# Kernel tuning notes

Hardware: AMD Instinct MI355X
Metric: run time of the kernel (lower is better)

Reference implementation:

```python
import jax, jax.numpy as jnp
import numpy as np

B, S, H, NH = 4, 2048, 1024, 16
HD = H // NH

def setup_inputs() -> dict:
    key = jax.random.key(0)
    ks = jax.random.split(key, 11)
    std = 1.0 / np.sqrt(H)
    inp = {
        'query': jax.random.normal(ks[0], (B, S, H), dtype=jnp.float32),
        'key':   jax.random.normal(ks[1], (B, S, H), dtype=jnp.float32),
        'value': jax.random.normal(ks[2], (B, S, H), dtype=jnp.float32),
        'Wq': jax.random.uniform(ks[3], (H, H), jnp.float32, -std, std),
        'bq': jax.random.uniform(ks[4], (H,), jnp.float32, -std, std),
        'Wk': jax.random.uniform(ks[5], (H, H), jnp.float32, -std, std),
        'bk': jax.random.uniform(ks[6], (H,), jnp.float32, -std, std),
        'Wv': jax.random.uniform(ks[7], (H, H), jnp.float32, -std, std),
        'bv': jax.random.uniform(ks[8], (H,), jnp.float32, -std, std),
        'Wo': jax.random.uniform(ks[9], (H, H), jnp.float32, -std, std),
        'bo': jax.random.uniform(ks[10], (H,), jnp.float32, -std, std),
    }
    return inp

def reference(query, key, value, Wq, bq, Wk, bk, Wv, bv, Wo, bo):
    def split_heads(x):  # [B,S,H] -> [B,NH,S,HD]
        return x.reshape(B, -1, NH, HD).transpose(0, 2, 1, 3)
    Q = split_heads(query @ Wq.T + bq)
    K = split_heads(key @ Wk.T + bk)
    V = split_heads(value @ Wv.T + bv)
    scores = jnp.einsum('bhqd,bhkd->bhqk', Q, K) / np.sqrt(HD).astype(np.float32)
    weights = jax.nn.softmax(scores, axis=-1)
    attn = jnp.einsum('bhqk,bhkd->bhqd', weights, V)  # [B,NH,S,HD]
    attn = attn.transpose(0, 2, 1, 3).reshape(B, -1, H)
    return attn @ Wo.T + bo
```

## Files before the change

### kernel.cpp

```cpp
#include <hip/hip_runtime.h>
#include <hip/hip_bf16.h>

typedef __attribute__((ext_vector_type(4)))  float f32x4;
typedef __attribute__((ext_vector_type(16))) float f32x16;
typedef __attribute__((ext_vector_type(8)))  short bf16x8;
typedef __attribute__((ext_vector_type(4)))  short bf16x4;

#define DEVI static __device__ __forceinline__
#define WAITV(N) asm volatile("s_waitcnt vmcnt(" #N ")" ::: "memory")
#define BAR() __builtin_amdgcn_s_barrier()
#define SCHEDB() __builtin_amdgcn_sched_barrier(0)

constexpr int Bn = 4, Sn = 2048, Hn = 1024, NHn = 16, HDn = 64;
constexpr int Kn = 1024, Nn = 1024;
constexpr float QSCALE = 0.18033688011112042f;

DEVI unsigned short f2bf(float x) {
    union { float f; unsigned u; } v; v.f = x;
    unsigned r = v.u + 0x7fffu + ((v.u >> 16) & 1u);
    return (unsigned short)(r >> 16);
}

DEVI f32x4 mfma16(bf16x8 a, bf16x8 b, f32x4 c) {
    return __builtin_amdgcn_mfma_f32_16x16x32_bf16(a, b, c, 0, 0, 0);
}
DEVI f32x16 mfma32(bf16x8 a, bf16x8 b, f32x16 c) {
    return __builtin_amdgcn_mfma_f32_32x32x16_bf16(a, b, c, 0, 0, 0);
}
DEVI unsigned cvt_pk_bf16(float lo, float hi) {
    unsigned r;
    asm("v_cvt_pk_bf16_f32 %0, %1, %2" : "=v"(r) : "v"(lo), "v"(hi));
    return r;
}
DEVI void pl32swap(unsigned &a, unsigned &b) {
    asm("v_permlane32_swap_b32 %0, %1" : "+v"(a), "+v"(b));
}
DEVI float exp2_raw(float x) { return __builtin_amdgcn_exp2f(x); }

typedef const __attribute__((address_space(1))) void* gas1_t;
typedef __attribute__((address_space(3))) void* gas3_t;

__global__ void convert_w_kernel(const float* __restrict__ w0, const float* __restrict__ w1,
                                 const float* __restrict__ w2, const float* __restrict__ w3,
                                 unsigned short* __restrict__ out)
{
    int mat = blockIdx.x >> 10;
    int i4  = ((blockIdx.x & 1023) << 8) + threadIdx.x;
    const float* w = mat == 0 ? w0 : mat == 1 ? w1 : mat == 2 ? w2 : w3;
    f32x4 v = *reinterpret_cast<const f32x4*>(w + (size_t)i4 * 4);
    union { unsigned u[2]; bf16x4 s; } pk;
    pk.u[0] = cvt_pk_bf16(v[0], v[1]);
    pk.u[1] = cvt_pk_bf16(v[2], v[3]);
    *reinterpret_cast<bf16x4*>(out + (((size_t)mat) << 20) + (size_t)i4 * 4) = pk.s;
}

__global__ __launch_bounds__(256, 2)
void out_proj_kernel(const unsigned short* __restrict__ Aw, const unsigned short* __restrict__ Bw,
                     const float* __restrict__ bias, float* __restrict__ Out)
{
    __shared__ __align__(16) unsigned short As[128 * 32];
    __shared__ __align__(16) unsigned short Bs[128 * 32];

    const int tid = threadIdx.x;
    const int wid = tid >> 6, lane = tid & 63;
    const int lhi = lane >> 4, llo = lane & 15;
    const int bid = blockIdx.x;
    const int sid = (bid & 7) * 64 + (bid >> 3);
    const int bx = sid & 7, by = sid >> 3;
    const int brow = by * 128, bcol = bx * 128;
    const int wr = wid >> 1, wc = wid & 1;

    f32x4 acc[4][4] = {};

    for (int kt = 0; kt < Kn / 32; ++kt) {
        __syncthreads();
        #pragma unroll
        for (int r = 0; r < 2; ++r) {
            int lin = r * 256 + tid;
            int row = lin >> 2, kc = (lin & 3) * 8;
            __builtin_amdgcn_global_load_lds(
                (gas1_t)(Bw + (size_t)(bcol + row) * Kn + kt * 32 + kc),
                (gas3_t)(Bs + (size_t)(r * 256 + wid * 64) * 8), 16, 0, 0);
        }
        #pragma unroll
        for (int r = 0; r < 2; ++r) {
            int lin = r * 256 + tid;
            int row = lin >> 2, kc = (lin & 3) * 8;
            __builtin_amdgcn_global_load_lds(
                (gas1_t)(Aw + (size_t)(brow + row) * Kn + kt * 32 + kc),
                (gas3_t)(As + (size_t)(r * 256 + wid * 64) * 8), 16, 0, 0);
        }
        __syncthreads();

        bf16x8 a[4], b[4];
        #pragma unroll
        for (int m = 0; m < 4; ++m)
            a[m] = *reinterpret_cast<const bf16x8*>(As + (wr * 64 + m * 16 + llo) * 32 + lhi * 8);
        #pragma unroll
        for (int n = 0; n < 4; ++n)
            b[n] = *reinterpret_cast<const bf16x8*>(Bs + (wc * 64 + n * 16 + llo) * 32 + lhi * 8);
        #pragma unroll
        for (int m = 0; m < 4; ++m)
            #pragma unroll
            for (int n = 0; n < 4; ++n)
                acc[m][n] = mfma16(a[m], b[n], acc[m][n]);
    }

    #pragma unroll
    for (int m = 0; m < 4; ++m)
        #pragma unroll
        for (int n = 0; n < 4; ++n) {
            const int col  = bcol + wc * 64 + n * 16 + llo;
            const int row0 = brow + wr * 64 + m * 16 + lhi * 4;
            const float bv = bias[col];
            #pragma unroll
            for (int r = 0; r < 4; ++r)
                Out[(size_t)(row0 + r) * Nn + col] = acc[m][n][r] + bv;
        }
}

__global__ __launch_bounds__(256, 2)
void qkv_proj_kernel(const float* __restrict__ xq, const float* __restrict__ xk,
                     const float* __restrict__ xv, const unsigned short* __restrict__ Wb,
                     const float* __restrict__ bq, const float* __restrict__ bk,
                     const float* __restrict__ bv,
                     unsigned short* __restrict__ Qw, unsigned short* __restrict__ Kw,
                     unsigned short* __restrict__ Vw)
{
    __shared__ __align__(16) unsigned short As[2][128 * 32];
    __shared__ __align__(16) unsigned short Bs[2][128 * 32];

    const int z = blockIdx.z;
    const float* A           = z == 0 ? xq : z == 1 ? xk : xv;
    const unsigned short* W  = Wb + (((size_t)z) << 20);
    const float* bias        = z == 0 ? bq : z == 1 ? bk : bv;
    unsigned short* Out      = z == 0 ? Qw : z == 1 ? Kw : Vw;
    const float scale        = z == 0 ? QSCALE : 1.0f;

    const int tid = threadIdx.x;
    const int wid = tid >> 6, lane = tid & 63;
    const int lhi = lane >> 4, llo = lane & 15;
    const int bid = blockIdx.x;
    const int sid = (bid & 7) * 64 + (bid >> 3);
    const int bx = sid & 7, by = sid >> 3;
    const int brow = by * 128, bcol = bx * 128;
    const int wr = wid >> 1, wc = wid & 1;

    f32x4 acc[4][4] = {};

    auto issueA = [&](f32x4 (&ar)[4], int kt) {
        #pragma unroll
        for (int r = 0; r < 4; ++r) {
            int lin = r * 256 + tid;
            int row = lin >> 3, kc = (lin & 7) * 4;
            ar[r] = *reinterpret_cast<const f32x4*>(A + (size_t)(brow + row) * Kn + kt * 32 + kc);
        }
    };
    auto stageB = [&](int buf, int kt) {
        #pragma unroll
        for (int r = 0; r < 2; ++r) {
            int lin = r * 256 + tid;
            int row = lin >> 2, kc = (lin & 3) * 8;
            __builtin_amdgcn_global_load_lds(
                (gas1_t)(W + (size_t)(bcol + row) * Kn + kt * 32 + kc),
                (gas3_t)(Bs[buf] + (size_t)(r * 256 + wid * 64) * 8), 16, 0, 0);
        }
    };
    auto writeA = [&](int buf, f32x4 (&ar)[4]) {
        #pragma unroll
        for (int r = 0; r < 4; ++r) {
            int lin = r * 256 + tid;
            int row = lin >> 3, kc = (lin & 7) * 4;
            union { unsigned u[2]; bf16x4 s; } pk;
            pk.u[0] = cvt_pk_bf16(ar[r][0], ar[r][1]);
            pk.u[1] = cvt_pk_bf16(ar[r][2], ar[r][3]);
            *reinterpret_cast<bf16x4*>(As[buf] + row * 32 + kc) = pk.s;
        }
    };
    auto compute = [&](int buf) {
        bf16x8 a[4], b[4];
        #pragma unroll
        for (int m = 0; m < 4; ++m)
            a[m] = *reinterpret_cast<const bf16x8*>(As[buf] + (wr * 64 + m * 16 + llo) * 32 + lhi * 8);
        #pragma unroll
        for (int n = 0; n < 4; ++n)
            b[n] = *reinterpret_cast<const bf16x8*>(Bs[buf] + (wc * 64 + n * 16 + llo) * 32 + lhi * 8);
        #pragma unroll
        for (int m = 0; m < 4; ++m)
            #pragma unroll
            for (int n = 0; n < 4; ++n)
                acc[m][n] = mfma16(a[m], b[n], acc[m][n]);
    };

    constexpr int NKT = Kn / 32;
    f32x4 ar0[4], ar1[4];

    issueA(ar0, 0);
    stageB(0, 0);
    writeA(0, ar0);
    __syncthreads();

    for (int kt = 0; kt < NKT; kt += 2) {
        issueA(ar1, kt + 1);
        stageB(1, kt + 1);
        compute(0);
        writeA(1, ar1);
        __syncthreads();
        if (kt + 2 < NKT) { issueA(ar0, kt + 2); stageB(0, kt + 2); }
        compute(1);
        if (kt + 2 < NKT) writeA(0, ar0);
        __syncthreads();
    }

    #pragma unroll
    for (int m = 0; m < 4; ++m) {
        #pragma unroll
        for (int n = 0; n < 4; ++n) {
            const int col  = bcol + wc * 64 + n * 16 + llo;
            const int row0 = brow + wr * 64 + m * 16 + lhi * 4;
            const float bv = bias[col];
            const int hh = col >> 6, d = col & 63;
            if (z != 2) {
                unsigned short* O = (unsigned short*)Out;
                #pragma unroll
                for (int r = 0; r < 4; ++r) {
                    int rowm = row0 + r;
                    int bb = rowm >> 11, ss = rowm & 2047;
                    O[((((size_t)bb * NHn + hh) * Sn + ss) << 6) + d] =
                        f2bf((acc[m][n][r] + bv) * scale);
                }
            } else {
                unsigned short* O = (unsigned short*)Out;
                const int bb = row0 >> 11, ss = row0 & 2047;
                union { unsigned u[2]; bf16x4 s; } pk;
                pk.u[0] = cvt_pk_bf16(acc[m][n][0] + bv, acc[m][n][1] + bv);
                pk.u[1] = cvt_pk_bf16(acc[m][n][2] + bv, acc[m][n][3] + bv);
                *reinterpret_cast<bf16x4*>(O + (((size_t)bb * NHn + hh) * HDn + d) * Sn + ss) = pk.s;
            }
        }
    }
}

__global__ __launch_bounds__(256, 2)
void attn_kernel(const unsigned short* __restrict__ Q, const unsigned short* __restrict__ K,
                 const unsigned short* __restrict__ Vt, unsigned short* __restrict__ On)
{
    __shared__ __align__(16) unsigned short LDST[3 * 8192];

    const int tid = threadIdx.x;
    const int wid = tid >> 6, lane = tid & 63;
    const int l31 = lane & 31, h = lane >> 5;
    const int bid = blockIdx.x;
    const int sid = (bid & 7) * 64 + (bid >> 3);
    const int bh = sid >> 3;
    const int qt = sid & 7;
    const int q0 = qt * 256 + wid * 64;

    const unsigned short* Qb = Q + (size_t)bh * Sn * HDn;
    const unsigned short* Kb = K + (size_t)bh * Sn * HDn;
    const unsigned short* Vb = Vt + (size_t)bh * HDn * Sn;

    int koff[2], voff[2];
    #pragma unroll
    for (int r = 0; r < 2; ++r) {
        int lin = (r * 256 + tid) * 16;
        int row = lin >> 7, colb = lin & 127;
        int scolb = colb ^ ((row & 7) << 4);
        koff[r] = row * HDn + (scolb >> 1);
        voff[r] = row * Sn + (scolb >> 1);
    }

    auto stage = [&](int bufEl, int key0) {
        #pragma unroll
        for (int r = 0; r < 2; ++r)
            __builtin_amdgcn_global_load_lds((gas1_t)(Kb + koff[r] + key0 * HDn),
                (gas3_t)(LDST + bufEl + r * 2048 + wid * 512), 16, 0, 0);
        #pragma unroll
        for (int r = 0; r < 2; ++r)
            __builtin_amdgcn_global_load_lds((gas1_t)(Vb + voff[r] + key0),
                (gas3_t)(LDST + bufEl + 4096 + r * 2048 + wid * 512), 16, 0, 0);
    };
    auto rdT = [&](int byteoff) -> bf16x8 {
        return *reinterpret_cast<const bf16x8*>((const char*)LDST + byteoff);
    };
    const int lrow = l31 * 128;
    const int lswz = (l31 & 7) << 4;

    bf16x8 qfA[4], qfB[4];
    #pragma unroll
    for (int sd = 0; sd < 4; ++sd) {
        qfA[sd] = *reinterpret_cast<const bf16x8*>(Qb + (size_t)(q0 + l31) * HDn + sd * 16 + h * 8);
        qfB[sd] = *reinterpret_cast<const bf16x8*>(Qb + (size_t)(q0 + 32 + l31) * HDn + sd * 16 + h * 8);
    }

    f32x16 oA0 = {}, oA1 = {}, oB0 = {}, oB1 = {};
    float lA = 0.f, lB = 0.f;

    auto body = [&](int base) {
        bf16x8 ka0[4], ka1[4];
        #pragma unroll
        for (int sd = 0; sd < 4; ++sd) {
            int la = lrow + ((sd * 32 + h * 16) ^ lswz);
            ka0[sd] = rdT(base + la);
            ka1[sd] = rdT(base + 4096 + la);
        }
        f32x16 sA0 = {}, sA1 = {}, sB0 = {}, sB1 = {};
        __builtin_amdgcn_s_setprio(1);
        #pragma unroll
        for (int sd = 0; sd < 4; ++sd) sA0 = mfma32(ka0[sd], qfA[sd], sA0);
        #pragma unroll
        for (int sd = 0; sd < 4; ++sd) sA1 = mfma32(ka1[sd], qfA[sd], sA1);
        #pragma unroll
        for (int sd = 0; sd < 4; ++sd) sB0 = mfma32(ka0[sd], qfB[sd], sB0);
        #pragma unroll
        for (int sd = 0; sd < 4; ++sd) sB1 = mfma32(ka1[sd], qfB[sd], sB1);
        __builtin_amdgcn_s_setprio(0);

        bf16x8 va0[4], va1[4];
        #pragma unroll
        for (int S = 0; S < 4; ++S) {
            int la = lrow + ((S * 32 + h * 16) ^ lswz);
            va0[S] = rdT(base + 8192 + la);
            va1[S] = rdT(base + 8192 + 4096 + la);
        }

        #pragma unroll
        for (int r = 0; r < 16; ++r) {
            sA0[r] = exp2_raw(sA0[r]); sA1[r] = exp2_raw(sA1[r]);
            sB0[r] = exp2_raw(sB0[r]); sB1[r] = exp2_raw(sB1[r]);
        }

        {
            float sa[16], sb[16];
            #pragma unroll
            for (int r = 0; r < 16; ++r) { sa[r] = sA0[r] + sA1[r]; sb[r] = sB0[r] + sB1[r]; }
            #pragma unroll
            for (int st = 8; st > 0; st >>= 1)
                #pragma unroll
                for (int r = 0; r < 8; ++r)
                    if (r < st) { sa[r] += sa[r + st]; sb[r] += sb[r + st]; }
            lA += sa[0];
            lB += sb[0];
        }

        unsigned WpA[2][4][2], WpB[2][4][2];
        #pragma unroll
        for (int R = 0; R < 4; ++R) {
            WpA[0][R][0] = cvt_pk_bf16(sA0[4 * R],     sA0[4 * R + 1]);
            WpA[0][R][1] = cvt_pk_bf16(sA0[4 * R + 2], sA0[4 * R + 3]);
            WpA[1][R][0] = cvt_pk_bf16(sA1[4 * R],     sA1[4 * R + 1]);
            WpA[1][R][1] = cvt_pk_bf16(sA1[4 * R + 2], sA1[4 * R + 3]);
            WpB[0][R][0] = cvt_pk_bf16(sB0[4 * R],     sB0[4 * R + 1]);
            WpB[0][R][1] = cvt_pk_bf16(sB0[4 * R + 2], sB0[4 * R + 3]);
            WpB[1][R][0] = cvt_pk_bf16(sB1[4 * R],     sB1[4 * R + 1]);
            WpB[1][R][1] = cvt_pk_bf16(sB1[4 * R + 2], sB1[4 * R + 3]);
        }

        #pragma unroll
        for (int kc = 0; kc < 2; ++kc) {
            #pragma unroll
            for (int sp = 0; sp < 2; ++sp) {
                const int S = kc * 2 + sp;
                unsigned a0 = WpA[kc][2 * sp][0], a2 = WpA[kc][2 * sp + 1][0];
                unsigned a1 = WpA[kc][2 * sp][1], a3 = WpA[kc][2 * sp + 1][1];
                pl32swap(a0, a2);
                pl32swap(a1, a3);
                union { unsigned u[4]; bf16x8 v; } pbA;
                pbA.u[0] = a0; pbA.u[1] = a1; pbA.u[2] = a2; pbA.u[3] = a3;
                unsigned b0 = WpB[kc][2 * sp][0], b2 = WpB[kc][2 * sp + 1][0];
                unsigned b1 = WpB[kc][2 * sp][1], b3 = WpB[kc][2 * sp + 1][1];
                pl32swap(b0, b2);
                pl32swap(b1, b3);
                union { unsigned u[4]; bf16x8 v; } pbB;
                pbB.u[0] = b0; pbB.u[1] = b1; pbB.u[2] = b2; pbB.u[3] = b3;
                __builtin_amdgcn_s_setprio(1);
                oA0 = mfma32(va0[S], pbA.v, oA0);
                oA1 = mfma32(va1[S], pbA.v, oA1);
                oB0 = mfma32(va0[S], pbB.v, oB0);
                oB1 = mfma32(va1[S], pbB.v, oB1);
                __builtin_amdgcn_s_setprio(0);
            }
        }
    };

    constexpr int NT = Sn / 64;
    stage(0, 0);
    int ec = 0, en = 8192, e2 = 16384;
    for (int n = 0; n < NT; ++n) {
        if (n + 1 < NT) {
            stage(en, (n + 1) * 64);
            WAITV(4);
        } else {
            WAITV(0);
        }
        BAR(); SCHEDB();
        body(ec * 2);
        int t = ec; ec = en; en = e2; e2 = t;
    }

    lA += __shfl_xor(lA, 32, 64);
    lB += __shfl_xor(lB, 32, 64);
    const float invA = 1.f / lA, invB = 1.f / lB;
    const int b = bh >> 4, hh = bh & 15;
    unsigned short* OrowA = On + ((size_t)b * Sn + (q0 + l31))      * Hn + hh * 64;
    unsigned short* OrowB = On + ((size_t)b * Sn + (q0 + 32 + l31)) * Hn + hh * 64;
    #pragma unroll
    for (int g = 0; g < 4; ++g) {
        union { unsigned u[2]; bf16x4 s; } pA0, pA1, pB0, pB1;
        pA0.u[0] = cvt_pk_bf16(oA0[4 * g] * invA,     oA0[4 * g + 1] * invA);
        pA0.u[1] = cvt_pk_bf16(oA0[4 * g + 2] * invA, oA0[4 * g + 3] * invA);
        pA1.u[0] = cvt_pk_bf16(oA1[4 * g] * invA,     oA1[4 * g + 1] * invA);
        pA1.u[1] = cvt_pk_bf16(oA1[4 * g + 2] * invA, oA1[4 * g + 3] * invA);
        pB0.u[0] = cvt_pk_bf16(oB0[4 * g] * invB,     oB0[4 * g + 1] * invB);
        pB0.u[1] = cvt_pk_bf16(oB0[4 * g + 2] * invB, oB0[4 * g + 3] * invB);
        pB1.u[0] = cvt_pk_bf16(oB1[4 * g] * invB,     oB1[4 * g + 1] * invB);
        pB1.u[1] = cvt_pk_bf16(oB1[4 * g + 2] * invB, oB1[4 * g + 3] * invB);
        *reinterpret_cast<bf16x4*>(OrowA + g * 8 + 4 * h)      = pA0.s;
        *reinterpret_cast<bf16x4*>(OrowA + 32 + g * 8 + 4 * h) = pA1.s;
        *reinterpret_cast<bf16x4*>(OrowB + g * 8 + 4 * h)      = pB0.s;
        *reinterpret_cast<bf16x4*>(OrowB + 32 + g * 8 + 4 * h) = pB1.s;
    }
}

extern "C" void kernel_launch(void* const* d_in, const int* in_sizes, int n_in,
                              void* d_out, int out_size, void* d_ws, size_t ws_size,
                              hipStream_t stream)
{
    (void)in_sizes; (void)n_in; (void)out_size;
    const float* q  = (const float*)d_in[0];
    const float* k  = (const float*)d_in[1];
    const float* v  = (const float*)d_in[2];
    const float* Wq = (const float*)d_in[3];
    const float* bq = (const float*)d_in[4];
    const float* Wk = (const float*)d_in[5];
    const float* bk = (const float*)d_in[6];
    const float* Wv = (const float*)d_in[7];
    const float* bv = (const float*)d_in[8];
    const float* Wo = (const float*)d_in[9];
    const float* bo = (const float*)d_in[10];
    float* out = (float*)d_out;

    if (ws_size < (size_t)72 * 1024 * 1024) return;

    unsigned short* Wb = (unsigned short*)d_ws;
    unsigned short* Qw = Wb + (size_t)4 * 1024 * 1024;
    unsigned short* Kw = Qw + (size_t)8 * 1024 * 1024;
    unsigned short* Vw = Kw + (size_t)8 * 1024 * 1024;
    unsigned short* Aw = Vw + (size_t)8 * 1024 * 1024;

    convert_w_kernel<<<4096, 256, 0, stream>>>(Wq, Wk, Wv, Wo, Wb);
    qkv_proj_kernel<<<dim3(512, 1, 3), 256, 0, stream>>>(q, k, v, Wb, bq, bk, bv, Qw, Kw, Vw);
    attn_kernel<<<512, 256, 0, stream>>>(Qw, Kw, Vw, Aw);
    out_proj_kernel<<<512, 256, 0, stream>>>(Aw, Wb + ((size_t)3 << 20), bo, out);
}
```

Baseline: 186.2 us.

## Stage fp32 activations directly into LDS with XOR swizzle in QKV projection

The QKV projection GEMM now loads the fp32 A tile straight into shared memory with global_load_lds, instead of going through registers and converting to bf16 before an LDS store. The bf16 conversion moves into the compute step. Both the A and B tiles use an XOR-swizzled chunk layout to reduce LDS bank conflicts, and the double-buffer loop becomes a simpler one-step prefetch. This removes register staging and VGPR pressure from the A path. In exchange, LDS usage and LDS read traffic for A double, and each A element is converted redundantly by both column waves.

Measured after the change: 186.3 us. About the same (+0.1%).

```diff
diff --git a/kernel.cpp b/kernel.cpp
--- a/kernel.cpp
+++ b/kernel.cpp
@@ -127,7 +127,7 @@
                      unsigned short* __restrict__ Qw, unsigned short* __restrict__ Kw,
                      unsigned short* __restrict__ Vw)
 {
-    __shared__ __align__(16) unsigned short As[2][128 * 32];
+    __shared__ __align__(16) float Af[2][128 * 32];
     __shared__ __align__(16) unsigned short Bs[2][128 * 32];
 
     const int z = blockIdx.z;
@@ -146,45 +146,56 @@
     const int brow = by * 128, bcol = bx * 128;
     const int wr = wid >> 1, wc = wid & 1;
 
+    const float* Ab          = A + (size_t)brow * Kn;
+    const unsigned short* Wp = W + (size_t)bcol * Kn;
+
     f32x4 acc[4][4] = {};
 
-    auto issueA = [&](f32x4 (&ar)[4], int kt) {
-        #pragma unroll
-        for (int r = 0; r < 4; ++r) {
-            int lin = r * 256 + tid;
-            int row = lin >> 3, kc = (lin & 7) * 4;
-            ar[r] = *reinterpret_cast<const f32x4*>(A + (size_t)(brow + row) * Kn + kt * 32 + kc);
-        }
+    int aoff[4], boff[2];
+    #pragma unroll
+    for (int r = 0; r < 4; ++r) {
+        int c = r * 256 + tid;
+        int row = c >> 3, u = c & 7;
+        aoff[r] = row * Kn + ((u ^ (row & 7)) << 2);
+    }
+    #pragma unroll
+    for (int r = 0; r < 2; ++r) {
+        int c = r * 256 + tid;
+        int row = c >> 2, u = c & 3;
+        boff[r] = row * Kn + ((u ^ (row & 3)) << 3);
+    }
+
+    auto stage = [&](int buf, int kt) {
+        #pragma unroll
+        for (int r = 0; r < 4; ++r)
+            __builtin_amdgcn_global_load_lds((gas1_t)(Ab + aoff[r] + kt * 32),
+                (gas3_t)(Af[buf] + (size_t)(r * 256 + wid * 64) * 4), 16, 0, 0);
+        #pragma unroll
+        for (int r = 0; r < 2; ++r)
+            __builtin_amdgcn_global_load_lds((gas1_t)(Wp + boff[r] + kt * 32),
+                (gas3_t)(Bs[buf] + (size_t)(r * 256 + wid * 64) * 8), 16, 0, 0);
     };
-    auto stageB = [&](int buf, int kt) {
-        #pragma unroll
-        for (int r = 0; r < 2; ++r) {
-            int lin = r * 256 + tid;
-            int row = lin >> 2, kc = (lin & 3) * 8;
-            __builtin_amdgcn_global_load_lds(
-                (gas1_t)(W + (size_t)(bcol + row) * Kn + kt * 32 + kc),
-                (gas3_t)(Bs[buf] + (size_t)(r * 256 + wid * 64) * 8), 16, 0, 0);
-        }
-    };
-    auto writeA = [&](int buf, f32x4 (&ar)[4]) {
-        #pragma unroll
-        for (int r = 0; r < 4; ++r) {
-            int lin = r * 256 + tid;
-            int row = lin >> 3, kc = (lin & 7) * 4;
-            union { unsigned u[2]; bf16x4 s; } pk;
-            pk.u[0] = cvt_pk_bf16(ar[r][0], ar[r][1]);
-            pk.u[1] = cvt_pk_bf16(ar[r][2], ar[r][3]);
-            *reinterpret_cast<bf16x4*>(As[buf] + row * 32 + kc) = pk.s;
-        }
-    };
+
     auto compute = [&](int buf) {
         bf16x8 a[4], b[4];
         #pragma unroll
-        for (int m = 0; m < 4; ++m)
-            a[m] = *reinterpret_cast<const bf16x8*>(As[buf] + (wr * 64 + m * 16 + llo) * 32 + lhi * 8);
-        #pragma unroll
-        for (int n = 0; n < 4; ++n)
-            b[n] = *reinterpret_cast<const bf16x8*>(Bs[buf] + (wc * 64 + n * 16 + llo) * 32 + lhi * 8);
+        for (int m = 0; m < 4; ++m) {
+            int row = wr * 64 + m * 16 + llo;
+            int s = row & 7;
+            f32x4 f0 = *reinterpret_cast<const f32x4*>(Af[buf] + row * 32 + (((lhi * 2)     ^ s) << 2));
+            f32x4 f1 = *reinterpret_cast<const f32x4*>(Af[buf] + row * 32 + (((lhi * 2 + 1) ^ s) << 2));
+            union { unsigned u[4]; bf16x8 v; } pa;
+            pa.u[0] = cvt_pk_bf16(f0[0], f0[1]);
+            pa.u[1] = cvt_pk_bf16(f0[2], f0[3]);
+            pa.u[2] = cvt_pk_bf16(f1[0], f1[1]);
+            pa.u[3] = cvt_pk_bf16(f1[2], f1[3]);
+            a[m] = pa.v;
+        }
+        #pragma unroll
+        for (int n = 0; n < 4; ++n) {
+            int row = wc * 64 + n * 16 + llo;
+            b[n] = *reinterpret_cast<const bf16x8*>(Bs[buf] + row * 32 + ((lhi ^ (row & 3)) << 3));
+        }
         #pragma unroll
         for (int m = 0; m < 4; ++m)
             #pragma unroll
@@ -193,22 +204,11 @@
     };
 
     constexpr int NKT = Kn / 32;
-    f32x4 ar0[4], ar1[4];
-
-    issueA(ar0, 0);
-    stageB(0, 0);
-    writeA(0, ar0);
+    stage(0, 0);
     __syncthreads();
-
-    for (int kt = 0; kt < NKT; kt += 2) {
-        issueA(ar1, kt + 1);
-        stageB(1, kt + 1);
-        compute(0);
-        writeA(1, ar1);
-        __syncthreads();
-        if (kt + 2 < NKT) { issueA(ar0, kt + 2); stageB(0, kt + 2); }
-        compute(1);
-        if (kt + 2 < NKT) writeA(0, ar0);
+    for (int kt = 0; kt < NKT; ++kt) {
+        if (kt + 1 < NKT) stage((kt + 1) & 1, kt + 1);
+        compute(kt & 1);
         __syncthreads();
     }
 
```
